# Optimization experiments

Measured on AMD Instinct MI355X. Metric: run time of the kernel, lower is better.

Reference implementation:

```python
import jax, jax.numpy as jnp
import numpy as np

N_NODES = 100000
N_EDGES = 400000
D_IN = 128
D_OUT = 128
BN_EPS = 1e-5


def setup_inputs() -> dict:
    key = jax.random.key(0)
    k1, k2, k3, k4, k5 = jax.random.split(key, 5)
    n_feat = jax.random.normal(k1, (N_NODES, D_IN), dtype=jnp.float32)
    edge_index = jax.random.randint(k2, (2, N_EDGES), 0, N_NODES, dtype=jnp.int32)
    edge_weight = jnp.ones((N_EDGES,), dtype=jnp.float32)
    # learned params: BatchNorm1d affine + Linear(in, out, bias=False)
    gamma = jnp.ones((D_IN,), dtype=jnp.float32) + 0.1 * jax.random.normal(k3, (D_IN,), dtype=jnp.float32)
    beta = 0.1 * jax.random.normal(k4, (D_IN,), dtype=jnp.float32)
    W = jax.random.normal(k5, (D_OUT, D_IN), dtype=jnp.float32) * (1.0 / np.sqrt(D_IN))
    return {"n_feat": n_feat, "edge_index": edge_index, "edge_weight": edge_weight,
            "gamma": gamma, "beta": beta, "W": W}


def reference(n_feat, edge_index, edge_weight, gamma, beta, W):
    # BatchNorm1d (training-mode batch stats, biased variance) -> ReLU -> Linear (no bias)
    mu = jnp.mean(n_feat, axis=0)
    var = jnp.mean(jnp.square(n_feat - mu), axis=0)
    xh = (n_feat - mu) * jax.lax.rsqrt(var + BN_EPS)
    y = jax.nn.relu(gamma * xh + beta)
    h = y @ W.T  # [N, D_OUT]
    # sparse adjacency matmul: out[row] += w * h[col]
    row, col = edge_index[0], edge_index[1]
    msgs = h[col] * edge_weight[:, None]          # gather, [E, D_OUT]
    agg = jax.ops.segment_sum(msgs, row, num_segments=N_NODES)
    return h * h + agg
```

## Files before the change

kernel.cpp:

```cpp
#include <hip/hip_runtime.h>

#define N_NODES 100000
#define N_EDGES 400000
#define D 128
#define BN_EPS 1e-5f
#define ELL_CAP 32

#define NSTAT 64
#define CS_BLOCKS 625
#define CS_ITER 20

#define WS_STATS   0
#define WS_HB      (NSTAT * 256)
#define WS_DEG2    (WS_HB + N_NODES * D / 2)
#define WS_ELL2    (WS_DEG2 + N_NODES)
#define WS_ELL2_END (WS_ELL2 + N_NODES * ELL_CAP * 2)
#define WS_WB      WS_ELL2_END
#define WS_SCL     (WS_WB + 8192)
#define WS_SHF     (WS_SCL + 128)
#define WS_ELL_END2 (WS_SHF + 128)
#define WS_SCALE   (NSTAT * 256)
#define WS_SHIFT   (WS_SCALE + 128)
#define WS_WT      (WS_SHIFT + 128)
#define WS_H       (WS_WT + D * D)
#define WS_DEG     (WS_H + N_NODES * D)
#define WS_ROWPTR  (WS_DEG + N_NODES)
#define WS_CURSOR  (WS_ROWPTR + N_NODES + 1)
#define WS_CSRCOL  (WS_CURSOR + N_NODES)
#define WS_CSRW    (WS_CSRCOL + N_EDGES)
#define WS_END     (WS_CSRW + N_EDGES)

typedef __attribute__((ext_vector_type(8))) short short8;
typedef __attribute__((ext_vector_type(4))) float f32x4;

static __device__ __forceinline__ unsigned short f2bf(float f) {
    union { float f; unsigned u; } v; v.f = f;
    unsigned r = v.u + 0x7FFF + ((v.u >> 16) & 1);
    return (unsigned short)(r >> 16);
}
static __device__ __forceinline__ float bf2f(unsigned short b) {
    union { unsigned u; float f; } v; v.u = ((unsigned)b) << 16;
    return v.f;
}

__global__ __launch_bounds__(256) void colstats_kernel(const float* __restrict__ x,
                                                       float* __restrict__ stats,
                                                       int* __restrict__ deg) {
    int tid = blockIdx.x * 256 + threadIdx.x;
    if (deg && tid < N_NODES) deg[tid] = 0;
    const int NTH = CS_BLOCKS * 256;
    const float4* x4 = (const float4*)x;
    float4 v[CS_ITER];
    #pragma unroll
    for (int i = 0; i < CS_ITER; i++) v[i] = x4[tid + i * NTH];
    float4 s = {0.f, 0.f, 0.f, 0.f};
    float4 q = {0.f, 0.f, 0.f, 0.f};
    #pragma unroll
    for (int i = 0; i < CS_ITER; i++) {
        s.x += v[i].x; s.y += v[i].y; s.z += v[i].z; s.w += v[i].w;
        q.x += v[i].x * v[i].x; q.y += v[i].y * v[i].y;
        q.z += v[i].z * v[i].z; q.w += v[i].w * v[i].w;
    }

    __shared__ float4 ss[256];
    __shared__ float4 sq[256];
    ss[threadIdx.x] = s;
    sq[threadIdx.x] = q;
    __syncthreads();
    if (threadIdx.x < 32) {
        float4 a = ss[threadIdx.x];
        float4 b = sq[threadIdx.x];
        for (int i = 32; i < 256; i += 32) {
            float4 t1 = ss[threadIdx.x + i];
            float4 t2 = sq[threadIdx.x + i];
            a.x += t1.x; a.y += t1.y; a.z += t1.z; a.w += t1.w;
            b.x += t2.x; b.y += t2.y; b.z += t2.z; b.w += t2.w;
        }
        float* st = stats + (blockIdx.x % NSTAT) * 256;
        int colb = (threadIdx.x * 4) & 127;
        atomicAdd(&st[colb + 0], a.x);
        atomicAdd(&st[colb + 1], a.y);
        atomicAdd(&st[colb + 2], a.z);
        atomicAdd(&st[colb + 3], a.w);
        atomicAdd(&st[128 + colb + 0], b.x);
        atomicAdd(&st[128 + colb + 1], b.y);
        atomicAdd(&st[128 + colb + 2], b.z);
        atomicAdd(&st[128 + colb + 3], b.w);
    }
}

__global__ __launch_bounds__(256) void fill_ell2_kernel(const int* __restrict__ ei,
                                                        const float* __restrict__ ew,
                                                        int* __restrict__ deg,
                                                        int2* __restrict__ ell2) {
    int e = blockIdx.x * 256 + threadIdx.x;
    if (e >= N_EDGES) return;
    int r = ei[e];
    int c = ei[N_EDGES + e];
    float w = ew[e];
    int slot = atomicAdd(&deg[r], 1);
    if (slot < ELL_CAP) ell2[r * ELL_CAP + slot] = make_int2(c, __float_as_int(w));
}

__global__ __launch_bounds__(256) void convw_finalize_kernel(const float* __restrict__ W,
                                                             const float* __restrict__ stats,
                                                             const float* __restrict__ gamma,
                                                             const float* __restrict__ beta,
                                                             unsigned short* __restrict__ Wb,
                                                             float* __restrict__ scale,
                                                             float* __restrict__ shift) {
    int b = blockIdx.x;
    int t = threadIdx.x;
    if (b < 16) {
        int i = b * 256 + t;
        float4 v = *(const float4*)(W + i * 4);
        ushort4 o;
        o.x = f2bf(v.x); o.y = f2bf(v.y); o.z = f2bf(v.z); o.w = f2bf(v.w);
        *(ushort4*)(Wb + i * 4) = o;
    } else if (t < 128) {
        float sum = 0.f, sq = 0.f;
        #pragma unroll 16
        for (int c = 0; c < NSTAT; c++) {
            sum += stats[c * 256 + t];
            sq  += stats[c * 256 + 128 + t];
        }
        float mu  = sum * (1.0f / N_NODES);
        float var = sq * (1.0f / N_NODES) - mu * mu;
        float sc  = gamma[t] * rsqrtf(var + BN_EPS);
        scale[t] = sc;
        shift[t] = beta[t] - mu * sc;
    }
}

#define YPAD 136
__global__ __launch_bounds__(256, 4) void gemm_mfma3_kernel(const float* __restrict__ x,
                                                            const float* __restrict__ scale,
                                                            const float* __restrict__ shift,
                                                            const unsigned short* __restrict__ Wb,
                                                            unsigned short* __restrict__ hb,
                                                            float* __restrict__ out) {
    __shared__ __align__(16) unsigned short Yl[64 * YPAD];
    int t = threadIdx.x;
    int row0 = blockIdx.x * 64;

    {
        int c4 = (t & 31) * 4;
        float4 sc = *(const float4*)(scale + c4);
        float4 sh = *(const float4*)(shift + c4);
        #pragma unroll
        for (int p = 0; p < 8; p++) {
            int i = t + p * 256;
            int r = i >> 5;
            int grow = row0 + r;
            int srow = grow < N_NODES ? grow : N_NODES - 1;
            float4 v = *(const float4*)(x + (size_t)srow * D + c4);
            ushort4 y;
            y.x = f2bf(fmaxf(fmaf(v.x, sc.x, sh.x), 0.f));
            y.y = f2bf(fmaxf(fmaf(v.y, sc.y, sh.y), 0.f));
            y.z = f2bf(fmaxf(fmaf(v.z, sc.z, sh.z), 0.f));
            y.w = f2bf(fmaxf(fmaf(v.w, sc.w, sh.w), 0.f));
            *(ushort4*)(Yl + r * YPAD + c4) = y;
        }
    }
    __syncthreads();

    int lane = t & 63;
    int wave = t >> 6;
    int m16  = lane & 15;
    int quad = lane >> 4;
    int wrow0 = wave * 16;

    f32x4 acc[8];
    #pragma unroll
    for (int nt = 0; nt < 8; nt++) acc[nt] = (f32x4){0.f, 0.f, 0.f, 0.f};

    const unsigned short* wb = Wb + m16 * D + quad * 8;
    const unsigned short* yl = Yl + (wrow0 + m16) * YPAD + quad * 8;
    #pragma unroll
    for (int kc = 0; kc < 4; kc++) {
        short8 a = *(const short8*)(yl + kc * 32);
        #pragma unroll
        for (int nt = 0; nt < 8; nt++) {
            short8 b = *(const short8*)(wb + nt * 16 * D + kc * 32);
            acc[nt] = __builtin_amdgcn_mfma_f32_16x16x32_bf16(a, b, acc[nt], 0, 0, 0);
        }
    }

    #pragma unroll
    for (int r = 0; r < 4; r++) {
        int grow = row0 + wrow0 + quad * 4 + r;
        if (grow < N_NODES) {
            float* orow = out + (size_t)grow * D + m16;
            unsigned short* hrow = hb + (size_t)grow * D + m16;
            #pragma unroll
            for (int nt = 0; nt < 8; nt++) {
                float v = acc[nt][r];
                orow[nt * 16] = v * v;
                hrow[nt * 16] = f2bf(v);
            }
        }
    }
}

__global__ __launch_bounds__(256) void gather_ell2_kernel(const int* __restrict__ deg,
                                                          const int2* __restrict__ ell2,
                                                          const unsigned short* __restrict__ hb,
                                                          float* __restrict__ out) {
    int lane = threadIdx.x & 15;
    int n = blockIdx.x * 16 + (threadIdx.x >> 4);
    if (n >= N_NODES) return;
    int dg = deg[n];
    if (dg > ELL_CAP) dg = ELL_CAP;
    int dg16 = dg < 16 ? dg : 16;

    int2 my = make_int2(0, 0);
    if (lane < dg16) my = ell2[n * ELL_CAP + lane];

    float acc[8] = {0.f, 0.f, 0.f, 0.f, 0.f, 0.f, 0.f, 0.f};
    int s = 0;
    for (; s + 4 <= dg16; s += 4) {
        int   c0 = __shfl(my.x, s + 0, 16); float w0 = __int_as_float(__shfl(my.y, s + 0, 16));
        int   c1 = __shfl(my.x, s + 1, 16); float w1 = __int_as_float(__shfl(my.y, s + 1, 16));
        int   c2 = __shfl(my.x, s + 2, 16); float w2 = __int_as_float(__shfl(my.y, s + 2, 16));
        int   c3 = __shfl(my.x, s + 3, 16); float w3 = __int_as_float(__shfl(my.y, s + 3, 16));
        short8 v0 = *(const short8*)(hb + (size_t)c0 * D + lane * 8);
        short8 v1 = *(const short8*)(hb + (size_t)c1 * D + lane * 8);
        short8 v2 = *(const short8*)(hb + (size_t)c2 * D + lane * 8);
        short8 v3 = *(const short8*)(hb + (size_t)c3 * D + lane * 8);
        #pragma unroll
        for (int j = 0; j < 8; j++) {
            acc[j] = fmaf(w0, bf2f((unsigned short)v0[j]), acc[j]);
            acc[j] = fmaf(w1, bf2f((unsigned short)v1[j]), acc[j]);
            acc[j] = fmaf(w2, bf2f((unsigned short)v2[j]), acc[j]);
            acc[j] = fmaf(w3, bf2f((unsigned short)v3[j]), acc[j]);
        }
    }
    for (; s < dg16; s++) {
        int c = __shfl(my.x, s, 16);
        float w = __int_as_float(__shfl(my.y, s, 16));
        short8 v = *(const short8*)(hb + (size_t)c * D + lane * 8);
        #pragma unroll
        for (int j = 0; j < 8; j++) acc[j] = fmaf(w, bf2f((unsigned short)v[j]), acc[j]);
    }
    for (s = 16; s < dg; s++) {
        int2 cw = ell2[n * ELL_CAP + s];
        float w = __int_as_float(cw.y);
        short8 v = *(const short8*)(hb + (size_t)cw.x * D + lane * 8);
        #pragma unroll
        for (int j = 0; j < 8; j++) acc[j] = fmaf(w, bf2f((unsigned short)v[j]), acc[j]);
    }

    float* o = out + (size_t)n * D + lane * 8;
    float4 a = *(const float4*)o;
    float4 b = *(const float4*)(o + 4);
    a.x += acc[0]; a.y += acc[1]; a.z += acc[2]; a.w += acc[3];
    b.x += acc[4]; b.y += acc[5]; b.z += acc[6]; b.w += acc[7];
    *(float4*)o = a;
    *(float4*)(o + 4) = b;
}

__global__ __launch_bounds__(128) void finalize_kernel(const float* __restrict__ stats,
                                                       const float* __restrict__ gamma,
                                                       const float* __restrict__ beta,
                                                       float* __restrict__ scale,
                                                       float* __restrict__ shift) {
    int d = threadIdx.x;
    float sum = 0.f, sq = 0.f;
    #pragma unroll 16
    for (int c = 0; c < NSTAT; c++) {
        sum += stats[c * 256 + d];
        sq  += stats[c * 256 + 128 + d];
    }
    float mu  = sum * (1.0f / N_NODES);
    float var = sq * (1.0f / N_NODES) - mu * mu;
    float sc  = gamma[d] * rsqrtf(var + BN_EPS);
    scale[d] = sc;
    shift[d] = beta[d] - mu * sc;
}

__global__ __launch_bounds__(256) void transposeW_kernel(const float* __restrict__ W,
                                                         float* __restrict__ Wt) {
    int i = blockIdx.x * blockDim.x + threadIdx.x;
    if (i < D * D) {
        int j = i >> 7;
        int k = i & 127;
        Wt[k * D + j] = W[i];
    }
}

template <int WRITE_SQ>
__global__ __launch_bounds__(256) void gemm_kernel(const float* __restrict__ x,
                                                   const float* __restrict__ scale,
                                                   const float* __restrict__ shift,
                                                   const float* __restrict__ Wt,
                                                   float* __restrict__ h,
                                                   float* __restrict__ out) {
    __shared__ float Ws[D * D];
    __shared__ float Ys[32 * D];
    int t = threadIdx.x;
    const float4* Wt4 = (const float4*)Wt;
    float4* Ws4 = (float4*)Ws;
    #pragma unroll 4
    for (int i = t; i < D * D / 4; i += 256) Ws4[i] = Wt4[i];
    int row0 = blockIdx.x * 32;
    const float4* x4 = (const float4*)(x + (size_t)row0 * D);
    float4* Ys4 = (float4*)Ys;
    #pragma unroll 2
    for (int i = t; i < 32 * D / 4; i += 256) {
        int c4 = (i & 31) * 4;
        float4 v = x4[i];
        v.x = fmaxf(fmaf(v.x, scale[c4 + 0], shift[c4 + 0]), 0.f);
        v.y = fmaxf(fmaf(v.y, scale[c4 + 1], shift[c4 + 1]), 0.f);
        v.z = fmaxf(fmaf(v.z, scale[c4 + 2], shift[c4 + 2]), 0.f);
        v.w = fmaxf(fmaf(v.w, scale[c4 + 3], shift[c4 + 3]), 0.f);
        Ys4[i] = v;
    }
    __syncthreads();
    int cg = t & 31;
    int rg = t >> 5;
    float4 acc[4] = {{0,0,0,0},{0,0,0,0},{0,0,0,0},{0,0,0,0}};
    #pragma unroll 2
    for (int k = 0; k < D; k += 4) {
        float4 w0 = *(const float4*)&Ws[(k + 0) * D + cg * 4];
        float4 w1 = *(const float4*)&Ws[(k + 1) * D + cg * 4];
        float4 w2 = *(const float4*)&Ws[(k + 2) * D + cg * 4];
        float4 w3 = *(const float4*)&Ws[(k + 3) * D + cg * 4];
        #pragma unroll
        for (int r = 0; r < 4; r++) {
            float4 y = *(const float4*)&Ys[(rg * 4 + r) * D + k];
            acc[r].x = fmaf(y.x, w0.x, fmaf(y.y, w1.x, fmaf(y.z, w2.x, fmaf(y.w, w3.x, acc[r].x))));
            acc[r].y = fmaf(y.x, w0.y, fmaf(y.y, w1.y, fmaf(y.z, w2.y, fmaf(y.w, w3.y, acc[r].y))));
            acc[r].z = fmaf(y.x, w0.z, fmaf(y.y, w1.z, fmaf(y.z, w2.z, fmaf(y.w, w3.z, acc[r].z))));
            acc[r].w = fmaf(y.x, w0.w, fmaf(y.y, w1.w, fmaf(y.z, w2.w, fmaf(y.w, w3.w, acc[r].w))));
        }
    }
    #pragma unroll
    for (int r = 0; r < 4; r++) {
        size_t row = (size_t)row0 + rg * 4 + r;
        float4 v = acc[r];
        *(float4*)&h[row * D + cg * 4] = v;
        if (WRITE_SQ) {
            float4 sqv = {v.x * v.x, v.y * v.y, v.z * v.z, v.w * v.w};
            *(float4*)&out[row * D + cg * 4] = sqv;
        }
    }
}

__global__ __launch_bounds__(256) void hist_kernel(const int* __restrict__ ei,
                                                   int* __restrict__ deg) {
    int e = blockIdx.x * 256 + threadIdx.x;
    if (e < N_EDGES) atomicAdd(&deg[ei[e]], 1);
}

__global__ __launch_bounds__(1024) void scan_kernel(const int* __restrict__ deg,
                                                    int* __restrict__ row_ptr,
                                                    int* __restrict__ cursor) {
    __shared__ int part[1024];
    int t = threadIdx.x;
    const int CHUNK = 100;
    int base = t * CHUNK;
    int s = 0;
    if (base < N_NODES) {
        for (int i = 0; i < CHUNK; i++) s += deg[base + i];
    }
    part[t] = s;
    __syncthreads();
    for (int off = 1; off < 1024; off <<= 1) {
        int v = (t >= off) ? part[t - off] : 0;
        __syncthreads();
        part[t] += v;
        __syncthreads();
    }
    int pre = (t == 0) ? 0 : part[t - 1];
    if (base < N_NODES) {
        for (int i = 0; i < CHUNK; i++) {
            row_ptr[base + i] = pre;
            cursor[base + i] = pre;
            pre += deg[base + i];
        }
    }
    if (t == 1023) row_ptr[N_NODES] = part[1023];
}

__global__ __launch_bounds__(256) void fill_kernel(const int* __restrict__ ei,
                                                   const float* __restrict__ ew,
                                                   int* __restrict__ cursor,
                                                   int* __restrict__ csr_col,
                                                   float* __restrict__ csr_w) {
    int e = blockIdx.x * 256 + threadIdx.x;
    if (e >= N_EDGES) return;
    int r = ei[e];
    int c = ei[N_EDGES + e];
    int slot = atomicAdd(&cursor[r], 1);
    csr_col[slot] = c;
    csr_w[slot] = ew[e];
}

__global__ __launch_bounds__(256) void gather_kernel(const int* __restrict__ row_ptr,
                                                     const int* __restrict__ csr_col,
                                                     const float* __restrict__ csr_w,
                                                     const float* __restrict__ h,
                                                     float* __restrict__ out) {
    int lane = threadIdx.x & 31;
    int n = blockIdx.x * 8 + (threadIdx.x >> 5);
    if (n >= N_NODES) return;
    int s0 = row_ptr[n];
    int s1 = row_ptr[n + 1];
    float4 acc = {0.f, 0.f, 0.f, 0.f};
    for (int s = s0; s < s1; s++) {
        int c = csr_col[s];
        float w = csr_w[s];
        float4 v = *(const float4*)&h[(size_t)c * D + lane * 4];
        acc.x = fmaf(w, v.x, acc.x);
        acc.y = fmaf(w, v.y, acc.y);
        acc.z = fmaf(w, v.z, acc.z);
        acc.w = fmaf(w, v.w, acc.w);
    }
    float4 hv = *(const float4*)&h[(size_t)n * D + lane * 4];
    float4 o;
    o.x = fmaf(hv.x, hv.x, acc.x);
    o.y = fmaf(hv.y, hv.y, acc.y);
    o.z = fmaf(hv.z, hv.z, acc.z);
    o.w = fmaf(hv.w, hv.w, acc.w);
    *(float4*)&out[(size_t)n * D + lane * 4] = o;
}

__global__ __launch_bounds__(256) void scatter_kernel(const int* __restrict__ ei,
                                                      const float* __restrict__ ew,
                                                      const float* __restrict__ h,
                                                      float* __restrict__ out) {
    int lane = threadIdx.x & 31;
    int e = blockIdx.x * 8 + (threadIdx.x >> 5);
    if (e >= N_EDGES) return;
    int r = ei[e];
    int c = ei[N_EDGES + e];
    float w = ew[e];
    float4 v = *(const float4*)&h[(size_t)c * D + lane * 4];
    float* o = out + (size_t)r * D + lane * 4;
    atomicAdd(o + 0, v.x * w);
    atomicAdd(o + 1, v.y * w);
    atomicAdd(o + 2, v.z * w);
    atomicAdd(o + 3, v.w * w);
}

extern "C" void kernel_launch(void* const* d_in, const int* in_sizes, int n_in,
                              void* d_out, int out_size, void* d_ws, size_t ws_size,
                              hipStream_t stream) {
    const float* n_feat = (const float*)d_in[0];
    const int*   ei     = (const int*)d_in[1];
    const float* ew     = (const float*)d_in[2];
    const float* gamma  = (const float*)d_in[3];
    const float* beta   = (const float*)d_in[4];
    const float* W      = (const float*)d_in[5];
    float* out = (float*)d_out;

    float* ws    = (float*)d_ws;
    float* stats = ws + WS_STATS;

    bool ell_ok = ws_size >= (size_t)WS_ELL_END2 * sizeof(float);
    bool csr_ok = ws_size >= (size_t)WS_END * sizeof(float);

    hipMemsetAsync(stats, 0, NSTAT * 256 * sizeof(float), stream);

    if (ell_ok) {
        unsigned short* hb  = (unsigned short*)(ws + WS_HB);
        int*  deg  = (int*)ws + WS_DEG2;
        int2* ell2 = (int2*)((int*)ws + WS_ELL2);
        unsigned short* Wb = (unsigned short*)(ws + WS_WB);
        float* scl = ws + WS_SCL;
        float* shf = ws + WS_SHF;

        colstats_kernel<<<CS_BLOCKS, 256, 0, stream>>>(n_feat, stats, deg);
        fill_ell2_kernel<<<(N_EDGES + 255) / 256, 256, 0, stream>>>(ei, ew, deg, ell2);
        convw_finalize_kernel<<<17, 256, 0, stream>>>(W, stats, gamma, beta, Wb, scl, shf);
        gemm_mfma3_kernel<<<(N_NODES + 63) / 64, 256, 0, stream>>>(n_feat, scl, shf, Wb, hb, out);
        gather_ell2_kernel<<<(N_NODES + 15) / 16, 256, 0, stream>>>(deg, ell2, hb, out);
    } else if (csr_ok) {
        float* scale = ws + WS_SCALE;
        float* shift = ws + WS_SHIFT;
        float* Wt    = ws + WS_WT;
        float* h     = ws + WS_H;
        int*   deg     = (int*)ws + WS_DEG;
        int*   row_ptr = (int*)ws + WS_ROWPTR;
        int*   cursor  = (int*)ws + WS_CURSOR;
        int*   csr_col = (int*)ws + WS_CSRCOL;
        float* csr_w   = ws + WS_CSRW;

        colstats_kernel<<<CS_BLOCKS, 256, 0, stream>>>(n_feat, stats, nullptr);
        finalize_kernel<<<1, 128, 0, stream>>>(stats, gamma, beta, scale, shift);
        transposeW_kernel<<<64, 256, 0, stream>>>(W, Wt);
        hipMemsetAsync(deg, 0, N_NODES * sizeof(int), stream);
        gemm_kernel<0><<<N_NODES / 32, 256, 0, stream>>>(n_feat, scale, shift, Wt, h, out);
        hist_kernel<<<(N_EDGES + 255) / 256, 256, 0, stream>>>(ei, deg);
        scan_kernel<<<1, 1024, 0, stream>>>(deg, row_ptr, cursor);
        fill_kernel<<<(N_EDGES + 255) / 256, 256, 0, stream>>>(ei, ew, cursor, csr_col, csr_w);
        gather_kernel<<<(N_NODES + 7) / 8, 256, 0, stream>>>(row_ptr, csr_col, csr_w, h, out);
    } else {
        float* scale = ws + WS_SCALE;
        float* shift = ws + WS_SHIFT;
        float* Wt    = ws + WS_WT;
        float* h     = ws + WS_H;
        colstats_kernel<<<CS_BLOCKS, 256, 0, stream>>>(n_feat, stats, nullptr);
        finalize_kernel<<<1, 128, 0, stream>>>(stats, gamma, beta, scale, shift);
        transposeW_kernel<<<64, 256, 0, stream>>>(W, Wt);
        gemm_kernel<1><<<N_NODES / 32, 256, 0, stream>>>(n_feat, scale, shift, Wt, h, out);
        scatter_kernel<<<(N_EDGES + 7) / 8, 256, 0, stream>>>(ei, ew, h, out);
    }
}
```

Before: 201.9 us.

## Move h*h into gather, store h as fp16, preload W fragments in GEMM

The GEMM no longer writes the fp32 h*h output. It only stores h, now as fp16 instead of bf16. The gather kernel reads the node's own h row and computes h*h plus the aggregate, so the full fp32 read-modify-write of out goes away. The GEMM also issues its x loads and all W fragment loads into registers before the LDS transform, with launch bounds lowered to 2 blocks per CU. This cuts global traffic and overlaps loads, at the cost of higher register pressure and h*h now being computed from rounded fp16 h rather than fp32, which adds rounding error.

```diff
diff --git a/kernel.cpp b/kernel.cpp
--- a/kernel.cpp
+++ b/kernel.cpp
@@ -41,6 +41,14 @@
 static __device__ __forceinline__ float bf2f(unsigned short b) {
     union { unsigned u; float f; } v; v.u = ((unsigned)b) << 16;
     return v.f;
+}
+static __device__ __forceinline__ unsigned short f2h(float f) {
+    union { _Float16 h; unsigned short u; } v; v.h = (_Float16)f;
+    return v.u;
+}
+static __device__ __forceinline__ float h2f(unsigned short u) {
+    union { unsigned short u; _Float16 h; } v; v.u = u;
+    return (float)v.h;
 }
 
 __global__ __launch_bounds__(256) void colstats_kernel(const float* __restrict__ x,
@@ -133,56 +141,63 @@
 }
 
 #define YPAD 136
-__global__ __launch_bounds__(256, 4) void gemm_mfma3_kernel(const float* __restrict__ x,
+__global__ __launch_bounds__(256, 2) void gemm_mfma4_kernel(const float* __restrict__ x,
                                                             const float* __restrict__ scale,
                                                             const float* __restrict__ shift,
                                                             const unsigned short* __restrict__ Wb,
-                                                            unsigned short* __restrict__ hb,
-                                                            float* __restrict__ out) {
+                                                            unsigned short* __restrict__ hh) {
     __shared__ __align__(16) unsigned short Yl[64 * YPAD];
     int t = threadIdx.x;
     int row0 = blockIdx.x * 64;
-
-    {
-        int c4 = (t & 31) * 4;
-        float4 sc = *(const float4*)(scale + c4);
-        float4 sh = *(const float4*)(shift + c4);
-        #pragma unroll
-        for (int p = 0; p < 8; p++) {
-            int i = t + p * 256;
-            int r = i >> 5;
-            int grow = row0 + r;
-            int srow = grow < N_NODES ? grow : N_NODES - 1;
-            float4 v = *(const float4*)(x + (size_t)srow * D + c4);
-            ushort4 y;
-            y.x = f2bf(fmaxf(fmaf(v.x, sc.x, sh.x), 0.f));
-            y.y = f2bf(fmaxf(fmaf(v.y, sc.y, sh.y), 0.f));
-            y.z = f2bf(fmaxf(fmaf(v.z, sc.z, sh.z), 0.f));
-            y.w = f2bf(fmaxf(fmaf(v.w, sc.w, sh.w), 0.f));
-            *(ushort4*)(Yl + r * YPAD + c4) = y;
-        }
-    }
-    __syncthreads();
-
     int lane = t & 63;
     int wave = t >> 6;
     int m16  = lane & 15;
     int quad = lane >> 4;
     int wrow0 = wave * 16;
+    int c4 = (t & 31) * 4;
+
+    float4 sc = *(const float4*)(scale + c4);
+    float4 sh = *(const float4*)(shift + c4);
+    float4 xv[8];
+    #pragma unroll
+    for (int p = 0; p < 8; p++) {
+        int r = (t + p * 256) >> 5;
+        int grow = row0 + r;
+        int srow = grow < N_NODES ? grow : N_NODES - 1;
+        xv[p] = *(const float4*)(x + (size_t)srow * D + c4);
+    }
+    const unsigned short* wb = Wb + m16 * D + quad * 8;
+    short8 bfr[4][8];
+    #pragma unroll
+    for (int kc = 0; kc < 4; kc++) {
+        #pragma unroll
+        for (int nt = 0; nt < 8; nt++) {
+            bfr[kc][nt] = *(const short8*)(wb + nt * 16 * D + kc * 32);
+        }
+    }
+    #pragma unroll
+    for (int p = 0; p < 8; p++) {
+        int r = (t + p * 256) >> 5;
+        ushort4 y;
+        y.x = f2bf(fmaxf(fmaf(xv[p].x, sc.x, sh.x), 0.f));
+        y.y = f2bf(fmaxf(fmaf(xv[p].y, sc.y, sh.y), 0.f));
+        y.z = f2bf(fmaxf(fmaf(xv[p].z, sc.z, sh.z), 0.f));
+        y.w = f2bf(fmaxf(fmaf(xv[p].w, sc.w, sh.w), 0.f));
+        *(ushort4*)(Yl + r * YPAD + c4) = y;
+    }
+    __syncthreads();
 
     f32x4 acc[8];
     #pragma unroll
     for (int nt = 0; nt < 8; nt++) acc[nt] = (f32x4){0.f, 0.f, 0.f, 0.f};
 
-    const unsigned short* wb = Wb + m16 * D + quad * 8;
     const unsigned short* yl = Yl + (wrow0 + m16) * YPAD + quad * 8;
     #pragma unroll
     for (int kc = 0; kc < 4; kc++) {
         short8 a = *(const short8*)(yl + kc * 32);
         #pragma unroll
         for (int nt = 0; nt < 8; nt++) {
-            short8 b = *(const short8*)(wb + nt * 16 * D + kc * 32);
-            acc[nt] = __builtin_amdgcn_mfma_f32_16x16x32_bf16(a, b, acc[nt], 0, 0, 0);
+            acc[nt] = __builtin_amdgcn_mfma_f32_16x16x32_bf16(a, bfr[kc][nt], acc[nt], 0, 0, 0);
         }
     }
 
@@ -190,25 +205,23 @@
     for (int r = 0; r < 4; r++) {
         int grow = row0 + wrow0 + quad * 4 + r;
         if (grow < N_NODES) {
-            float* orow = out + (size_t)grow * D + m16;
-            unsigned short* hrow = hb + (size_t)grow * D + m16;
+            unsigned short* hrow = hh + (size_t)grow * D + m16;
             #pragma unroll
             for (int nt = 0; nt < 8; nt++) {
-                float v = acc[nt][r];
-                orow[nt * 16] = v * v;
-                hrow[nt * 16] = f2bf(v);
+                hrow[nt * 16] = f2h(acc[nt][r]);
             }
         }
     }
 }
 
-__global__ __launch_bounds__(256) void gather_ell2_kernel(const int* __restrict__ deg,
+__global__ __launch_bounds__(256) void gather_ell3_kernel(const int* __restrict__ deg,
                                                           const int2* __restrict__ ell2,
-                                                          const unsigned short* __restrict__ hb,
+                                                          const unsigned short* __restrict__ hh,
                                                           float* __restrict__ out) {
     int lane = threadIdx.x & 15;
     int n = blockIdx.x * 16 + (threadIdx.x >> 4);
     if (n >= N_NODES) return;
+    short8 hself = *(const short8*)(hh + (size_t)n * D + lane * 8);
     int dg = deg[n];
     if (dg > ELL_CAP) dg = ELL_CAP;
     int dg16 = dg < 16 ? dg : 16;
@@ -223,38 +236,45 @@
         int   c1 = __shfl(my.x, s + 1, 16); float w1 = __int_as_float(__shfl(my.y, s + 1, 16));
         int   c2 = __shfl(my.x, s + 2, 16); float w2 = __int_as_float(__shfl(my.y, s + 2, 16));
         int   c3 = __shfl(my.x, s + 3, 16); float w3 = __int_as_float(__shfl(my.y, s + 3, 16));
-        short8 v0 = *(const short8*)(hb + (size_t)c0 * D + lane * 8);
-        short8 v1 = *(const short8*)(hb + (size_t)c1 * D + lane * 8);
-        short8 v2 = *(const short8*)(hb + (size_t)c2 * D + lane * 8);
-        short8 v3 = *(const short8*)(hb + (size_t)c3 * D + lane * 8);
+        short8 v0 = *(const short8*)(hh + (size_t)c0 * D + lane * 8);
+        short8 v1 = *(const short8*)(hh + (size_t)c1 * D + lane * 8);
+        short8 v2 = *(const short8*)(hh + (size_t)c2 * D + lane * 8);
+        short8 v3 = *(const short8*)(hh + (size_t)c3 * D + lane * 8);
         #pragma unroll
         for (int j = 0; j < 8; j++) {
-            acc[j] = fmaf(w0, bf2f((unsigned short)v0[j]), acc[j]);
-            acc[j] = fmaf(w1, bf2f((unsigned short)v1[j]), acc[j]);
-            acc[j] = fmaf(w2, bf2f((unsigned short)v2[j]), acc[j]);
-            acc[j] = fmaf(w3, bf2f((unsigned short)v3[j]), acc[j]);
+            acc[j] = fmaf(w0, h2f((unsigned short)v0[j]), acc[j]);
+            acc[j] = fmaf(w1, h2f((unsigned short)v1[j]), acc[j]);
+            acc[j] = fmaf(w2, h2f((unsigned short)v2[j]), acc[j]);
+            acc[j] = fmaf(w3, h2f((unsigned short)v3[j]), acc[j]);
         }
     }
     for (; s < dg16; s++) {
         int c = __shfl(my.x, s, 16);
         float w = __int_as_float(__shfl(my.y, s, 16));
-        short8 v = *(const short8*)(hb + (size_t)c * D + lane * 8);
+        short8 v = *(const short8*)(hh + (size_t)c * D + lane * 8);
         #pragma unroll
-        for (int j = 0; j < 8; j++) acc[j] = fmaf(w, bf2f((unsigned short)v[j]), acc[j]);
+        for (int j = 0; j < 8; j++) acc[j] = fmaf(w, h2f((unsigned short)v[j]), acc[j]);
     }
     for (s = 16; s < dg; s++) {
         int2 cw = ell2[n * ELL_CAP + s];
         float w = __int_as_float(cw.y);
-        short8 v = *(const short8*)(hb + (size_t)cw.x * D + lane * 8);
+        short8 v = *(const short8*)(hh + (size_t)cw.x * D + lane * 8);
         #pragma unroll
-        for (int j = 0; j < 8; j++) acc[j] = fmaf(w, bf2f((unsigned short)v[j]), acc[j]);
-    }
-
+        for (int j = 0; j < 8; j++) acc[j] = fmaf(w, h2f((unsigned short)v[j]), acc[j]);
+    }
+
+    float4 a, b;
+    {
+        float h0 = h2f((unsigned short)hself[0]); float h1 = h2f((unsigned short)hself[1]);
+        float h2 = h2f((unsigned short)hself[2]); float h3 = h2f((unsigned short)hself[3]);
+        float h4 = h2f((unsigned short)hself[4]); float h5 = h2f((unsigned short)hself[5]);
+        float h6 = h2f((unsigned short)hself[6]); float h7 = h2f((unsigned short)hself[7]);
+        a.x = fmaf(h0, h0, acc[0]); a.y = fmaf(h1, h1, acc[1]);
+        a.z = fmaf(h2, h2, acc[2]); a.w = fmaf(h3, h3, acc[3]);
+        b.x = fmaf(h4, h4, acc[4]); b.y = fmaf(h5, h5, acc[5]);
+        b.z = fmaf(h6, h6, acc[6]); b.w = fmaf(h7, h7, acc[7]);
+    }
     float* o = out + (size_t)n * D + lane * 8;
-    float4 a = *(const float4*)o;
-    float4 b = *(const float4*)(o + 4);
-    a.x += acc[0]; a.y += acc[1]; a.z += acc[2]; a.w += acc[3];
-    b.x += acc[4]; b.y += acc[5]; b.z += acc[6]; b.w += acc[7];
     *(float4*)o = a;
     *(float4*)(o + 4) = b;
 }
@@ -463,7 +483,7 @@
     hipMemsetAsync(stats, 0, NSTAT * 256 * sizeof(float), stream);
 
     if (ell_ok) {
-        unsigned short* hb  = (unsigned short*)(ws + WS_HB);
+        unsigned short* hh  = (unsigned short*)(ws + WS_HB);
         int*  deg  = (int*)ws + WS_DEG2;
         int2* ell2 = (int2*)((int*)ws + WS_ELL2);
         unsigned short* Wb = (unsigned short*)(ws + WS_WB);
@@ -473,8 +493,8 @@
         colstats_kernel<<<CS_BLOCKS, 256, 0, stream>>>(n_feat, stats, deg);
         fill_ell2_kernel<<<(N_EDGES + 255) / 256, 256, 0, stream>>>(ei, ew, deg, ell2);
         convw_finalize_kernel<<<17, 256, 0, stream>>>(W, stats, gamma, beta, Wb, scl, shf);
-        gemm_mfma3_kernel<<<(N_NODES + 63) / 64, 256, 0, stream>>>(n_feat, scl, shf, Wb, hb, out);
-        gather_ell2_kernel<<<(N_NODES + 15) / 16, 256, 0, stream>>>(deg, ell2, hb, out);
+        gemm_mfma4_kernel<<<(N_NODES + 63) / 64, 256, 0, stream>>>(n_feat, scl, shf, Wb, hh);
+        gather_ell3_kernel<<<(N_NODES + 15) / 16, 256, 0, stream>>>(deg, ell2, hh, out);
     } else if (csr_ok) {
         float* scale = ws + WS_SCALE;
         float* shift = ws + WS_SHIFT;
```

Result: faster. 195.1 us (-3.4%).
